# Kernel optimization log

Measured on AMD Instinct MI355X. Metric: run time of the kernel, lower is better.

Reference implementation:

```python
import jax, jax.numpy as jnp
import numpy as np

B, N, K, D = 4, 8192, 16, 128
G = D // 4  # spatial-encoding groups, 4 feature channels each ('a4')
BN_EPS = 1e-5


def setup_inputs() -> dict:
    key = jax.random.key(0)
    ks = jax.random.split(key, 8)
    x = jax.random.normal(ks[0], (B, N, D), jnp.float32)
    xyz = jax.random.uniform(ks[1], (B, N, 3), jnp.float32)
    knn = jax.random.randint(ks[2], (B, N, K), 0, N)
    proj_w = jax.random.normal(ks[3], (D, D), jnp.float32) * 0.02  # nn.Linear(in,out,bias=False) weight [out,in]
    coor = jax.random.normal(ks[4], (G * 3,), jnp.float32) * 0.5   # init_coor(out_dim//4).flatten()
    scale = jnp.full((G,), 0.1, jnp.float32)                        # zeros + 0.1
    bn_weight = jnp.ones((D,), jnp.float32)                          # init=1.0
    bn_bias = jnp.zeros((D,), jnp.float32)
    return dict(x=x, xyz=xyz, knn=knn, proj_w=proj_w, coor=coor,
                scale=scale, bn_weight=bn_weight, bn_bias=bn_bias)


def reference(x, xyz, knn, proj_w, coor, scale, bn_weight, bn_bias):
    Bb, Nn, _ = x.shape
    # 1) linear projection (no bias)
    h = jnp.einsum('bnc,dc->bnd', x, proj_w)  # [B,N,D]
    # 2) learned spatial position encoding weights: (4, G) = [cx,cy,cz,scale^2]
    w = jnp.concatenate([coor.reshape(-1, 3).T, (scale * scale)[None, :]], axis=0)
    # 3) KNN gathers
    bidx = jnp.arange(Bb)[:, None, None]
    xyz_n = xyz[bidx, knn]                      # [B,N,K,3]
    rel = xyz_n - xyz[:, :, None, :]            # relative coords
    f4 = jnp.concatenate([rel, jnp.sum(rel * rel, axis=-1, keepdims=True)], axis=-1)  # [B,N,K,4]
    e = jnp.einsum('bnkf,fg->bnkg', f4, w)      # [B,N,K,G] encoding per group
    hn = h[bidx, knn]                           # [B,N,K,D] neighbor features
    # 4) add encoding per group of 4 channels, max-aggregate over K neighbors
    g = hn.reshape(Bb, Nn, K, G, 4) + e[..., None]
    agg = jnp.max(g, axis=2).reshape(Bb, Nn, D)
    # 5) BatchNorm1d over B*N rows (training-mode batch stats, biased var)
    flat = agg.reshape(-1, D)
    mean = jnp.mean(flat, axis=0)
    var = jnp.mean(jnp.square(flat - mean), axis=0)
    y = (flat - mean) * jax.lax.rsqrt(var + BN_EPS) * bn_weight + bn_bias
    return y.reshape(Bb, Nn, D)
```

## Files before the change

kernel.cpp:

```cpp
#include <hip/hip_runtime.h>
#include <math.h>

#define BB 4
#define NN 8192
#define KK 16
#define DD 128
#define NPTS (BB * NN)
#define FBLOCKS 1024
#define BPX 128
#define PAD 16
#define BN_EPS 1e-5f

__global__ void transpose_w(const float* __restrict__ w, float* __restrict__ wt) {
    int i = blockIdx.x * 256 + threadIdx.x;
    int d = i >> 7;
    int c = i & 127;
    wt[c * 128 + d] = w[d * 128 + c];
}

__global__ __launch_bounds__(256) void gemm_h(const float* __restrict__ x,
                                              const float* __restrict__ wt,
                                              float* __restrict__ h) {
    __shared__ float xs[32][128];
    const int block_row = blockIdx.x * 32;
    const int t = threadIdx.x;

    const float4* xg = reinterpret_cast<const float4*>(x + (size_t)block_row * 128);
    float4* xs4 = reinterpret_cast<float4*>(&xs[0][0]);
#pragma unroll
    for (int i = 0; i < 4; ++i) xs4[t + 256 * i] = xg[t + 256 * i];
    __syncthreads();

    const int ty = t >> 5;
    const int tx = t & 31;
    const int r0 = ty * 4;
    const int c0 = tx * 4;

    float acc[4][4];
#pragma unroll
    for (int r = 0; r < 4; ++r)
#pragma unroll
        for (int j = 0; j < 4; ++j) acc[r][j] = 0.f;

    for (int c4 = 0; c4 < 32; ++c4) {
        float4 wv[4];
#pragma unroll
        for (int j = 0; j < 4; ++j)
            wv[j] = *reinterpret_cast<const float4*>(wt + (size_t)(c4 * 4 + j) * 128 + c0);
#pragma unroll
        for (int r = 0; r < 4; ++r) {
            float4 xv = *reinterpret_cast<const float4*>(&xs[r0 + r][c4 * 4]);
            const float xc[4] = {xv.x, xv.y, xv.z, xv.w};
#pragma unroll
            for (int j = 0; j < 4; ++j) {
                acc[r][0] = fmaf(xc[j], wv[j].x, acc[r][0]);
                acc[r][1] = fmaf(xc[j], wv[j].y, acc[r][1]);
                acc[r][2] = fmaf(xc[j], wv[j].z, acc[r][2]);
                acc[r][3] = fmaf(xc[j], wv[j].w, acc[r][3]);
            }
        }
    }

#pragma unroll
    for (int r = 0; r < 4; ++r) {
        float4 o = make_float4(acc[r][0], acc[r][1], acc[r][2], acc[r][3]);
        *reinterpret_cast<float4*>(h + (size_t)(block_row + r0 + r) * 128 + c0) = o;
    }
}

__global__ __launch_bounds__(256, 4) void fused_gbn(const float* __restrict__ h,
                                                    const float* __restrict__ xyz,
                                                    const int* __restrict__ knn,
                                                    const float* __restrict__ coor,
                                                    const float* __restrict__ scale,
                                                    const float* __restrict__ bnw,
                                                    const float* __restrict__ bnb,
                                                    float* __restrict__ out,
                                                    float* gacc,
                                                    int* cntx,
                                                    int* cntg,
                                                    int* genx) {
    const int t = threadIdx.x;
    const int g = t & 31;
    const int sub = t >> 5;

    const int xcd = blockIdx.x & 7;
    const int jj = blockIdx.x >> 3;
    const int slot = ((xcd & 1) << 7) + jj;
    const int b = xcd >> 1;
    const int pbase = (b << 13) + (slot << 5);

    const float c0w = coor[g * 3 + 0];
    const float c1w = coor[g * 3 + 1];
    const float c2w = coor[g * 3 + 2];
    const float sg = scale[g];
    const float s2 = sg * sg;

    float lsum[4] = {0.f, 0.f, 0.f, 0.f};
    float lsq[4]  = {0.f, 0.f, 0.f, 0.f};
    float4 accv[4];

#pragma unroll
    for (int it = 0; it < 4; ++it) {
        const int p = pbase + it * 8 + sub;
        const float* ctr = xyz + (size_t)p * 3;
        const float cx = ctr[0], cy = ctr[1], cz = ctr[2];
        const int* kn = knn + (size_t)p * KK;

        float4 acc = make_float4(-INFINITY, -INFINITY, -INFINITY, -INFINITY);

#pragma unroll
        for (int k = 0; k < KK; ++k) {
            const int idx = kn[k];
            const int row = (b << 13) + idx;
            const float* nb = xyz + (size_t)row * 3;
            const float rx = nb[0] - cx;
            const float ry = nb[1] - cy;
            const float rz = nb[2] - cz;
            const float r2 = rx * rx + ry * ry + rz * rz;
            const float e = rx * c0w + ry * c1w + rz * c2w + r2 * s2;
            const float4 hv = *reinterpret_cast<const float4*>(h + (size_t)row * 128 + g * 4);
            acc.x = fmaxf(acc.x, hv.x + e);
            acc.y = fmaxf(acc.y, hv.y + e);
            acc.z = fmaxf(acc.z, hv.z + e);
            acc.w = fmaxf(acc.w, hv.w + e);
        }

        accv[it] = acc;
        lsum[0] += acc.x; lsum[1] += acc.y; lsum[2] += acc.z; lsum[3] += acc.w;
        lsq[0] += acc.x * acc.x; lsq[1] += acc.y * acc.y;
        lsq[2] += acc.z * acc.z; lsq[3] += acc.w * acc.w;
    }

    __shared__ float red[8][128];
    float sink = 0.f;
#pragma unroll
    for (int j = 0; j < 4; ++j) red[sub][g * 4 + j] = lsum[j];
    __syncthreads();
    if (t < 128) {
        float s = 0.f;
#pragma unroll
        for (int s8 = 0; s8 < 8; ++s8) s += red[s8][t];
        sink += __hip_atomic_fetch_add(&gacc[t * PAD], s,
                                       __ATOMIC_RELAXED, __HIP_MEMORY_SCOPE_AGENT);
    }
    __syncthreads();
#pragma unroll
    for (int j = 0; j < 4; ++j) red[sub][g * 4 + j] = lsq[j];
    __syncthreads();
    if (t < 128) {
        float q = 0.f;
#pragma unroll
        for (int s8 = 0; s8 < 8; ++s8) q += red[s8][t];
        sink += __hip_atomic_fetch_add(&gacc[(128 + t) * PAD], q,
                                       __ATOMIC_RELAXED, __HIP_MEMORY_SCOPE_AGENT);
    }
    asm volatile("" :: "v"(sink));
    __syncthreads();

    if (t == 0) {
        int prev = __hip_atomic_fetch_add(&cntx[xcd * PAD], 1,
                                          __ATOMIC_RELAXED, __HIP_MEMORY_SCOPE_AGENT);
        if (prev == BPX - 1) {
            int gprev = __hip_atomic_fetch_add(cntg, 1,
                                               __ATOMIC_RELAXED, __HIP_MEMORY_SCOPE_AGENT);
            if (gprev == 7) {
#pragma unroll
                for (int xx = 0; xx < 8; ++xx)
                    __hip_atomic_store(&genx[xx * PAD], 1,
                                       __ATOMIC_RELAXED, __HIP_MEMORY_SCOPE_SYSTEM);
            }
        }
        while (__hip_atomic_load(&genx[xcd * PAD],
                                 __ATOMIC_RELAXED, __HIP_MEMORY_SCOPE_SYSTEM) == 0) {
            __builtin_amdgcn_s_sleep(32);
        }
    }
    __syncthreads();

    __shared__ float sA[128], sC[128];
    if (t < 128) {
        const float stot = __hip_atomic_load(&gacc[t * PAD],
                                             __ATOMIC_RELAXED, __HIP_MEMORY_SCOPE_SYSTEM);
        const float qtot = __hip_atomic_load(&gacc[(128 + t) * PAD],
                                             __ATOMIC_RELAXED, __HIP_MEMORY_SCOPE_SYSTEM);
        const float inv_n = 1.0f / (float)NPTS;
        const float mean = stot * inv_n;
        const float var = qtot * inv_n - mean * mean;
        const float rstd = rsqrtf(var + BN_EPS);
        const float A = rstd * bnw[t];
        sA[t] = A;
        sC[t] = bnb[t] - mean * A;
    }
    __syncthreads();

    const float4 A4 = make_float4(sA[g * 4], sA[g * 4 + 1], sA[g * 4 + 2], sA[g * 4 + 3]);
    const float4 C4 = make_float4(sC[g * 4], sC[g * 4 + 1], sC[g * 4 + 2], sC[g * 4 + 3]);
#pragma unroll
    for (int it = 0; it < 4; ++it) {
        const int p = pbase + it * 8 + sub;
        float4 v = accv[it];
        v.x = fmaf(v.x, A4.x, C4.x);
        v.y = fmaf(v.y, A4.y, C4.y);
        v.z = fmaf(v.z, A4.z, C4.z);
        v.w = fmaf(v.w, A4.w, C4.w);
        *reinterpret_cast<float4*>(out + (size_t)p * 128 + g * 4) = v;
    }
}

extern "C" void kernel_launch(void* const* d_in, const int* in_sizes, int n_in,
                              void* d_out, int out_size, void* d_ws, size_t ws_size,
                              hipStream_t stream) {
    const float* x      = (const float*)d_in[0];
    const float* xyz    = (const float*)d_in[1];
    const int*   knn    = (const int*)d_in[2];
    const float* proj_w = (const float*)d_in[3];
    const float* coor   = (const float*)d_in[4];
    const float* scale  = (const float*)d_in[5];
    const float* bnw    = (const float*)d_in[6];
    const float* bnb    = (const float*)d_in[7];
    float* out = (float*)d_out;

    char* ws = (char*)d_ws;
    size_t off = 0;
    float* h    = (float*)(ws + off); off += (size_t)NPTS * DD * 4;
    float* wt   = (float*)(ws + off); off += 65536;
    float* gacc = (float*)(ws + off);
    size_t atomic_base = off;
    off += 256 * PAD * 4;
    int* cntx = (int*)(ws + off); off += 8 * PAD * 4;
    int* cntg = (int*)(ws + off); off += PAD * 4;
    int* genx = (int*)(ws + off); off += 8 * PAD * 4;
    size_t atomic_bytes = off - atomic_base;

    hipMemsetAsync(gacc, 0, atomic_bytes, stream);

    transpose_w<<<64, 256, 0, stream>>>(proj_w, wt);
    gemm_h<<<NPTS / 32, 256, 0, stream>>>(x, wt, h);
    fused_gbn<<<FBLOCKS, 256, 0, stream>>>(h, xyz, knn, coor, scale, bnw, bnb,
                                           out, gacc, cntx, cntg, genx);
}
```

Before: 85.86 us.

## Fold memset into transpose, shrink GEMM tile, batch KNN gather loads

```diff
diff --git a/kernel.cpp b/kernel.cpp
--- a/kernel.cpp
+++ b/kernel.cpp
@@ -11,7 +11,16 @@
 #define PAD 16
 #define BN_EPS 1e-5f
 
-__global__ void transpose_w(const float* __restrict__ w, float* __restrict__ wt) {
+__global__ void transpose_w(const float* __restrict__ w, float* __restrict__ wt,
+                            float* gacc, int* cntx, int* cntg, int* genx) {
+    if (blockIdx.x == 0) {
+        for (int j = threadIdx.x; j < 256 * PAD; j += 256) gacc[j] = 0.f;
+        if (threadIdx.x < 8) {
+            cntx[threadIdx.x * PAD] = 0;
+            genx[threadIdx.x * PAD] = 0;
+        }
+        if (threadIdx.x == 0) *cntg = 0;
+    }
     int i = blockIdx.x * 256 + threadIdx.x;
     int d = i >> 7;
     int c = i & 127;
@@ -21,34 +30,35 @@
 __global__ __launch_bounds__(256) void gemm_h(const float* __restrict__ x,
                                               const float* __restrict__ wt,
                                               float* __restrict__ h) {
-    __shared__ float xs[32][128];
-    const int block_row = blockIdx.x * 32;
+    __shared__ float xs[16][128];
+    const int block_row = blockIdx.x * 16;
     const int t = threadIdx.x;
 
     const float4* xg = reinterpret_cast<const float4*>(x + (size_t)block_row * 128);
     float4* xs4 = reinterpret_cast<float4*>(&xs[0][0]);
 #pragma unroll
-    for (int i = 0; i < 4; ++i) xs4[t + 256 * i] = xg[t + 256 * i];
+    for (int i = 0; i < 2; ++i) xs4[t + 256 * i] = xg[t + 256 * i];
     __syncthreads();
 
     const int ty = t >> 5;
     const int tx = t & 31;
-    const int r0 = ty * 4;
+    const int r0 = ty * 2;
     const int c0 = tx * 4;
 
-    float acc[4][4];
-#pragma unroll
-    for (int r = 0; r < 4; ++r)
+    float acc[2][4];
+#pragma unroll
+    for (int r = 0; r < 2; ++r)
 #pragma unroll
         for (int j = 0; j < 4; ++j) acc[r][j] = 0.f;
 
+#pragma unroll 4
     for (int c4 = 0; c4 < 32; ++c4) {
         float4 wv[4];
 #pragma unroll
         for (int j = 0; j < 4; ++j)
             wv[j] = *reinterpret_cast<const float4*>(wt + (size_t)(c4 * 4 + j) * 128 + c0);
 #pragma unroll
-        for (int r = 0; r < 4; ++r) {
+        for (int r = 0; r < 2; ++r) {
             float4 xv = *reinterpret_cast<const float4*>(&xs[r0 + r][c4 * 4]);
             const float xc[4] = {xv.x, xv.y, xv.z, xv.w};
 #pragma unroll
@@ -62,7 +72,7 @@
     }
 
 #pragma unroll
-    for (int r = 0; r < 4; ++r) {
+    for (int r = 0; r < 2; ++r) {
         float4 o = make_float4(acc[r][0], acc[r][1], acc[r][2], acc[r][3]);
         *reinterpret_cast<float4*>(h + (size_t)(block_row + r0 + r) * 128 + c0) = o;
     }
@@ -89,6 +99,7 @@
     const int slot = ((xcd & 1) << 7) + jj;
     const int b = xcd >> 1;
     const int pbase = (b << 13) + (slot << 5);
+    const int rowbase = b << 13;
 
     const float c0w = coor[g * 3 + 0];
     const float c1w = coor[g * 3 + 1];
@@ -105,25 +116,45 @@
         const int p = pbase + it * 8 + sub;
         const float* ctr = xyz + (size_t)p * 3;
         const float cx = ctr[0], cy = ctr[1], cz = ctr[2];
-        const int* kn = knn + (size_t)p * KK;
+
+        const int4* kn4 = reinterpret_cast<const int4*>(knn + (size_t)p * KK);
+        const int4 ka = kn4[0], kb = kn4[1], kc = kn4[2], kd = kn4[3];
+        int rows[16];
+        rows[0] = rowbase + ka.x;  rows[1] = rowbase + ka.y;
+        rows[2] = rowbase + ka.z;  rows[3] = rowbase + ka.w;
+        rows[4] = rowbase + kb.x;  rows[5] = rowbase + kb.y;
+        rows[6] = rowbase + kb.z;  rows[7] = rowbase + kb.w;
+        rows[8] = rowbase + kc.x;  rows[9] = rowbase + kc.y;
+        rows[10] = rowbase + kc.z; rows[11] = rowbase + kc.w;
+        rows[12] = rowbase + kd.x; rows[13] = rowbase + kd.y;
+        rows[14] = rowbase + kd.z; rows[15] = rowbase + kd.w;
 
         float4 acc = make_float4(-INFINITY, -INFINITY, -INFINITY, -INFINITY);
 
 #pragma unroll
-        for (int k = 0; k < KK; ++k) {
-            const int idx = kn[k];
-            const int row = (b << 13) + idx;
-            const float* nb = xyz + (size_t)row * 3;
-            const float rx = nb[0] - cx;
-            const float ry = nb[1] - cy;
-            const float rz = nb[2] - cz;
-            const float r2 = rx * rx + ry * ry + rz * rz;
-            const float e = rx * c0w + ry * c1w + rz * c2w + r2 * s2;
-            const float4 hv = *reinterpret_cast<const float4*>(h + (size_t)row * 128 + g * 4);
-            acc.x = fmaxf(acc.x, hv.x + e);
-            acc.y = fmaxf(acc.y, hv.y + e);
-            acc.z = fmaxf(acc.z, hv.z + e);
-            acc.w = fmaxf(acc.w, hv.w + e);
+        for (int half = 0; half < 2; ++half) {
+            const int k0 = half * 8;
+            float4 hv[8];
+#pragma unroll
+            for (int k = 0; k < 8; ++k)
+                hv[k] = *reinterpret_cast<const float4*>(h + (size_t)rows[k0 + k] * 128 + g * 4);
+            float ep[8];
+#pragma unroll
+            for (int k = 0; k < 8; ++k) {
+                const float* nb = xyz + (size_t)rows[k0 + k] * 3;
+                const float rx = nb[0] - cx;
+                const float ry = nb[1] - cy;
+                const float rz = nb[2] - cz;
+                ep[k] = rx * c0w + ry * c1w + rz * c2w
+                      + (rx * rx + ry * ry + rz * rz) * s2;
+            }
+#pragma unroll
+            for (int k = 0; k < 8; ++k) {
+                acc.x = fmaxf(acc.x, hv[k].x + ep[k]);
+                acc.y = fmaxf(acc.y, hv[k].y + ep[k]);
+                acc.z = fmaxf(acc.z, hv[k].z + ep[k]);
+                acc.w = fmaxf(acc.w, hv[k].w + ep[k]);
+            }
         }
 
         accv[it] = acc;
@@ -225,18 +256,13 @@
     size_t off = 0;
     float* h    = (float*)(ws + off); off += (size_t)NPTS * DD * 4;
     float* wt   = (float*)(ws + off); off += 65536;
-    float* gacc = (float*)(ws + off);
-    size_t atomic_base = off;
-    off += 256 * PAD * 4;
+    float* gacc = (float*)(ws + off); off += 256 * PAD * 4;
     int* cntx = (int*)(ws + off); off += 8 * PAD * 4;
     int* cntg = (int*)(ws + off); off += PAD * 4;
     int* genx = (int*)(ws + off); off += 8 * PAD * 4;
-    size_t atomic_bytes = off - atomic_base;
-
-    hipMemsetAsync(gacc, 0, atomic_bytes, stream);
-
-    transpose_w<<<64, 256, 0, stream>>>(proj_w, wt);
-    gemm_h<<<NPTS / 32, 256, 0, stream>>>(x, wt, h);
+
+    transpose_w<<<64, 256, 0, stream>>>(proj_w, wt, gacc, cntx, cntg, genx);
+    gemm_h<<<NPTS / 16, 256, 0, stream>>>(x, wt, h);
     fused_gbn<<<FBLOCKS, 256, 0, stream>>>(h, xyz, knn, coor, scale, bnw, bnb,
                                            out, gacc, cntx, cntg, genx);
 }
```

Measured after the change: 99.46 us. 1.16x slower.
